# Optimization experiments

Measured on AMD Instinct MI355X. Metric: run time of the kernel, lower is better.

## Reference

```python
import jax, jax.numpy as jnp
import numpy as np

SIGMA = 5.67e-8  # Stefan-Boltzmann constant
NX = 13
N = NX * NX  # 169 nodes
B = 131072


def _build_matrices(L=0.1, thickness=0.001, board_k=15.0, emis=0.8):
    dx = L / (NX - 1)
    dy = L / (NX - 1)
    GLx = thickness * board_k * dy / dx
    GLy = thickness * board_k * dx / dy
    GR = 2.0 * dx * dy * emis
    iface = {0, NX - 1, NX * NX - 1, NX * NX - NX}
    K = np.zeros((N, N), dtype=np.float32)
    for j in range(NX):
        for i in range(NX):
            idn = i + NX * j
            if idn in iface:
                K[idn, idn] = 1.0
            else:
                gii = 0.0
                if i + 1 < NX:
                    K[idn, idn + 1] = -GLx  # east
                    gii += GLx
                if i - 1 >= 0:
                    K[idn, idn - 1] = -GLx  # west
                    gii += GLx
                if j + 1 < NX:
                    K[idn, idn + NX] = -GLx  # north (original code uses -GLx here too)
                    gii += GLy
                if j - 1 >= 0:
                    K[idn, idn - NX] = -GLx  # south (original code uses -GLx here too)
                    gii += GLy
                K[idn, idn] = gii
    e = np.full(N, GR, dtype=np.float32)
    for t in iface:
        e[t] = 0.0
    return jnp.asarray(K), jnp.asarray(e)


def setup_inputs() -> dict:
    key = jax.random.key(0)
    k1, k2, k3, k4 = jax.random.split(key, 4)
    # realistic temperatures (K) and heat loads (W)
    outputs = 270.0 + 60.0 * jax.random.uniform(k1, (B, NX, NX), dtype=jnp.float32)
    heaters = 0.5 * jax.random.uniform(k2, (B, NX, NX), dtype=jnp.float32)
    interfaces = 0.5 * jax.random.uniform(k3, (B, NX, NX), dtype=jnp.float32)
    Tenv = 270.0 + 30.0 * jax.random.uniform(k4, (B, 1), dtype=jnp.float32)
    K, e_diag = _build_matrices()
    return {"outputs": outputs, "heaters": heaters, "interfaces": interfaces,
            "Tenv": Tenv, "K": K, "e_diag": e_diag}


def reference(outputs, heaters, interfaces, Tenv, K, e_diag):
    b = outputs.shape[0]
    T = outputs.reshape(b, -1)                    # [B, 169]
    Q = heaters.reshape(b, -1) + interfaces.reshape(b, -1)  # [B, 169]
    # original computes K @ T_nodes_x_batch; batch-major equivalent is T @ K^T
    conduction = jnp.einsum('bn,mn->bm', T, K)    # [B, 169]
    radiation = SIGMA * e_diag[None, :] * (T ** 4 - Tenv ** 4)  # Tenv [B,1] broadcasts
    excess = conduction + radiation - Q
    return jnp.mean(jnp.abs(excess))
```

## Files before the change

kernel.cpp:

```cpp
#include <hip/hip_runtime.h>
#include <math.h>
#include <stdint.h>


#define SIGMA_F 5.67e-8f

constexpr int BLOCK = 256;
constexpr int TILE  = 2048;
constexpr int THALO = 16;
constexpr int TWIN  = TILE + 2 * THALO;

typedef float f4b __attribute__((ext_vector_type(4), aligned(16)));

static __device__ __forceinline__ void gl_lds16(const float* g, float* l) {
    __builtin_amdgcn_global_load_lds(
        (const __attribute__((address_space(1))) void*)g,
        (__attribute__((address_space(3))) void*)l, 16, 0, 0);
}

__global__ __launch_bounds__(256) void fused_residual_v9(
    const float* __restrict__ T,
    const float* __restrict__ H,
    const float* __restrict__ F,
    const float* __restrict__ Tenv,
    const float* __restrict__ K,
    const float* __restrict__ Ediag,
    float* __restrict__ partials,
    int total,
    int ntiles)
{
    __shared__ float sT[2][TWIN];
    __shared__ float sH[2][TILE];
    __shared__ float sF[2][TILE];
    __shared__ unsigned sTab[184];
    __shared__ float sred[BLOCK / 64];

    const float GLx = -K[1 * 169 + 2];
    const float GRs = SIGMA_F * Ediag[1];
    const int tid = (int)threadIdx.x;

    if (tid < 184) {
        int m = (tid < 169) ? tid : tid - 169;
        int ii = m % 13;
        unsigned cW = (ii > 0)  ? 1u : 0u;
        unsigned cE = (ii < 12) ? 1u : 0u;
        unsigned cN = (m < 156) ? 1u : 0u;
        unsigned cS = (m >= 13) ? 1u : 0u;
        sTab[tid] = cW | (cE << 8) | (cN << 16) | (cS << 24);
    }

    const int nb  = (int)gridDim.x;
    const int bid = (int)blockIdx.x;
    const int qd  = ntiles / nb, rem = ntiles % nb;
    const int t0  = bid * qd + (bid < rem ? bid : rem);
    const int nt  = qd + (bid < rem ? 1 : 0);

    float acc = 0.0f;

    auto STAGE = [&](int buf, int tile) {
        const int gb = tile * TILE;
        #pragma unroll
        for (int k = 0; k < 3; ++k) {
            const int c = tid + k * BLOCK;
            if (c < TWIN / 4) {
                int src = gb - THALO + c * 4;
                src = src < 0 ? 0 : src;
                src = src > total - 4 ? total - 4 : src;
                gl_lds16(T + src, &sT[buf][c * 4]);
            }
        }
        #pragma unroll
        for (int k = 0; k < 2; ++k) {
            const int c = tid + k * BLOCK;
            gl_lds16(H + gb + c * 4, &sH[buf][c * 4]);
            gl_lds16(F + gb + c * 4, &sF[buf][c * 4]);
        }
    };

    if (nt > 0) {
        STAGE(0, t0);
        __syncthreads();
        int cur = 0;
        for (int k = 0; k < nt; ++k) {
            if (k + 1 < nt) STAGE(cur ^ 1, t0 + k + 1);

            const int tb = (t0 + k) * TILE;
            const int e0 = tb + tid * 8;
            const int lb = THALO + tid * 8;
            const float* __restrict__ Tb = &sT[cur][0];

            f4b a0 = *(const f4b*)&Tb[lb];
            f4b a1 = *(const f4b*)&Tb[lb + 4];
            float s0 = Tb[lb - 13];
            f4b sA = *(const f4b*)&Tb[lb - 12];
            f4b sB = *(const f4b*)&Tb[lb - 8];
            float n0 = Tb[lb + 13], n1 = Tb[lb + 14], n2 = Tb[lb + 15];
            f4b nA = *(const f4b*)&Tb[lb + 16];
            float n7 = Tb[lb + 20];
            float tw = Tb[lb - 1], te = Tb[lb + 8];
            f4b h0v = *(const f4b*)&sH[cur][tid * 8];
            f4b h1v = *(const f4b*)&sH[cur][tid * 8 + 4];
            f4b f0v = *(const f4b*)&sF[cur][tid * 8];
            f4b f1v = *(const f4b*)&sF[cur][tid * 8 + 4];

            const float tC[8] = {a0.x, a0.y, a0.z, a0.w, a1.x, a1.y, a1.z, a1.w};
            const float sv[8] = {s0, sA.x, sA.y, sA.z, sA.w, sB.x, sB.y, sB.z};
            const float nv[8] = {n0, n1, n2, nA.x, nA.y, nA.z, nA.w, n7};
            const float qv[8] = {h0v.x + f0v.x, h0v.y + f0v.y,
                                 h0v.z + f0v.z, h0v.w + f0v.w,
                                 h1v.x + f1v.x, h1v.y + f1v.y,
                                 h1v.z + f1v.z, h1v.w + f1v.w};

            const unsigned ue = (unsigned)e0;
            const unsigned b0 = ue / 169u;
            const int m0 = (int)(ue - b0 * 169u);

            float tvA = Tenv[b0];
            float tvB = tvA;
            if (m0 >= 162) tvB = Tenv[b0 + 1];
            const float tv4A = (tvA * tvA) * (tvA * tvA);
            const float tv4B = (tvB * tvB) * (tvB * tvB);

            #pragma unroll
            for (int j = 0; j < 8; ++j) {
                const unsigned w = sTab[m0 + j];
                const float mW = (float)(w & 0xffu);
                const float mE = (float)((w >> 8) & 0xffu);
                const float mN = (float)((w >> 16) & 0xffu);
                const float mS = (float)(w >> 24);

                const float t  = tC[j];
                const float twv = (j == 0) ? tw : tC[j - 1];
                const float tev = (j == 7) ? te : tC[j + 1];
                float s = mW * twv;
                s = fmaf(mE, tev, s);
                s = fmaf(mN, nv[j], s);
                s = fmaf(mS, sv[j], s);
                const float nn = (mW + mE) + (mN + mS);
                const float q  = qv[j];
                const float tv4 = (m0 + j >= 169) ? tv4B : tv4A;
                const float t2 = t * t;
                const float d  = fmaf(t2, t2, -tv4);
                const float core = fmaf(GLx, fmaf(nn, t, -s), fmaf(GRs, d, -q));
                const float ex = (nn == 2.0f) ? (t - q) : core;
                acc += fabsf(ex);
            }

            __syncthreads();
            cur ^= 1;
        }
    }

    for (int e = ntiles * TILE + bid * BLOCK + tid; e < total;
         e += nb * BLOCK) {
        unsigned b = (unsigned)e / 169u;
        int m = e - (int)b * 169;
        int ii = m % 13;
        bool cE = (ii < 12), cW = (ii > 0), cN = (m < 156), cS = (m >= 13);
        bool ifc = (m == 0) | (m == 12) | (m == 156) | (m == 168);
        float t  = T[e];
        float s  = (cE ? T[e + 1] : 0.0f) + (cW ? T[e - 1] : 0.0f)
                 + (cN ? T[e + 13] : 0.0f) + (cS ? T[e - 13] : 0.0f);
        float nn = (float)((int)cE + (int)cW + (int)cN + (int)cS);
        float tv = Tenv[b];
        float tv4 = (tv * tv) * (tv * tv);
        float t2 = t * t, t4 = t2 * t2;
        float qq = H[e] + F[e];
        float ex = ifc ? (t - qq) : (GLx * (nn * t - s) + GRs * (t4 - tv4) - qq);
        acc += fabsf(ex);
    }

    #pragma unroll
    for (int off = 32; off > 0; off >>= 1)
        acc += __shfl_down(acc, off, 64);
    const int lane = tid & 63;
    const int wid  = tid >> 6;
    if (lane == 0) sred[wid] = acc;
    __syncthreads();
    if (tid == 0) {
        float s = 0.0f;
        #pragma unroll
        for (int w = 0; w < BLOCK / 64; ++w) s += sred[w];
        partials[bid] = s;
    }
}

__global__ __launch_bounds__(256) void finalize_kernel(
    const float* __restrict__ partials, int n,
    float* __restrict__ out, float inv_total)
{
    __shared__ float sred[BLOCK / 64];
    float acc = 0.0f;
    for (int i = (int)threadIdx.x; i < n; i += BLOCK) acc += partials[i];
    #pragma unroll
    for (int off = 32; off > 0; off >>= 1)
        acc += __shfl_down(acc, off, 64);
    int lane = threadIdx.x & 63;
    int wid  = threadIdx.x >> 6;
    if (lane == 0) sred[wid] = acc;
    __syncthreads();
    if (threadIdx.x == 0) {
        float s = 0.0f;
        #pragma unroll
        for (int w = 0; w < BLOCK / 64; ++w) s += sred[w];
        out[0] = s * inv_total;
    }
}

extern "C" void kernel_launch(void* const* d_in, const int* in_sizes, int n_in,
                              void* d_out, int out_size, void* d_ws, size_t ws_size,
                              hipStream_t stream) {
    const float* T    = (const float*)d_in[0];
    const float* H    = (const float*)d_in[1];
    const float* F    = (const float*)d_in[2];
    const float* Tenv = (const float*)d_in[3];
    const float* K    = (const float*)d_in[4];
    const float* E    = (const float*)d_in[5];
    float* out      = (float*)d_out;
    float* partials = (float*)d_ws;

    const int total  = in_sizes[0];
    const int ntiles = total / TILE;

    int grid = 768;
    if (grid > ntiles) grid = ntiles > 0 ? ntiles : 1;
    if ((size_t)grid * sizeof(float) > ws_size) grid = (int)(ws_size / sizeof(float));
    if (grid < 1) grid = 1;

    fused_residual_v9<<<grid, BLOCK, 0, stream>>>(T, H, F, Tenv, K, E, partials,
                                                  total, ntiles);

    const float inv_total = 1.0f / (float)total;
    finalize_kernel<<<1, BLOCK, 0, stream>>>(partials, grid, out, inv_total);
}
```

Baseline: 268.3 us.

## Give each wavefront its own double-buffered tile with vmcnt waits instead of block barriers

Each of the four wavefronts in a block now owns a private 512-element double-buffered LDS slice. It stages T (with halo), H, F and the needed Tenv values by async global-to-LDS loads, and waits on vmcnt counters instead of block-wide __syncthreads. Tenv is also prefetched into LDS rather than read with scattered global loads, and tiles are strided across all wavefronts in the grid. The aim is to remove block-level barrier stalls and let each wave overlap its own loads with compute. The cost is more halo overhead per element and reliance on hand-written waitcnt ordering.

```diff
diff --git a/kernel.cpp b/kernel.cpp
--- a/kernel.cpp
+++ b/kernel.cpp
@@ -1,24 +1,31 @@
 #include <hip/hip_runtime.h>
 #include <math.h>
-#include <stdint.h>
 
 
 #define SIGMA_F 5.67e-8f
 
 constexpr int BLOCK = 256;
-constexpr int TILE  = 2048;
-constexpr int THALO = 16;
-constexpr int TWIN  = TILE + 2 * THALO;
+constexpr int TILE  = 512;
+constexpr int HOFF  = 544;
+constexpr int FOFF  = 1056;
+constexpr int EOFF  = 1568;
+constexpr int SLICE = 1632;
+constexpr int WSTR  = 2 * SLICE;
 
 typedef float f4b __attribute__((ext_vector_type(4), aligned(16)));
 
-static __device__ __forceinline__ void gl_lds16(const float* g, float* l) {
+static __device__ __forceinline__ void gl16(const float* g, float* l) {
     __builtin_amdgcn_global_load_lds(
         (const __attribute__((address_space(1))) void*)g,
         (__attribute__((address_space(3))) void*)l, 16, 0, 0);
 }
-
-__global__ __launch_bounds__(256) void fused_residual_v9(
+static __device__ __forceinline__ void gl4(const float* g, float* l) {
+    __builtin_amdgcn_global_load_lds(
+        (const __attribute__((address_space(1))) void*)g,
+        (__attribute__((address_space(3))) void*)l, 4, 0, 0);
+}
+
+__global__ __launch_bounds__(256) void fused_residual_v12(
     const float* __restrict__ T,
     const float* __restrict__ H,
     const float* __restrict__ F,
@@ -26,18 +33,18 @@
     const float* __restrict__ K,
     const float* __restrict__ Ediag,
     float* __restrict__ partials,
-    int total,
-    int ntiles)
+    int total)
 {
-    __shared__ float sT[2][TWIN];
-    __shared__ float sH[2][TILE];
-    __shared__ float sF[2][TILE];
+    __shared__ float    S[4 * WSTR];
     __shared__ unsigned sTab[184];
-    __shared__ float sred[BLOCK / 64];
+    __shared__ float    sred[4];
+
+    const int tid  = (int)threadIdx.x;
+    const int lane = tid & 63;
+    const int wid  = tid >> 6;
 
     const float GLx = -K[1 * 169 + 2];
     const float GRs = SIGMA_F * Ediag[1];
-    const int tid = (int)threadIdx.x;
 
     if (tid < 184) {
         int m = (tid < 169) ? tid : tid - 169;
@@ -49,139 +56,137 @@
         sTab[tid] = cW | (cE << 8) | (cN << 16) | (cS << 24);
     }
 
-    const int nb  = (int)gridDim.x;
-    const int bid = (int)blockIdx.x;
-    const int qd  = ntiles / nb, rem = ntiles % nb;
-    const int t0  = bid * qd + (bid < rem ? bid : rem);
-    const int nt  = qd + (bid < rem ? 1 : 0);
-
     float acc = 0.0f;
-
-    auto STAGE = [&](int buf, int tile) {
-        const int gb = tile * TILE;
-        #pragma unroll
-        for (int k = 0; k < 3; ++k) {
-            const int c = tid + k * BLOCK;
-            if (c < TWIN / 4) {
-                int src = gb - THALO + c * 4;
-                src = src < 0 ? 0 : src;
-                src = src > total - 4 ? total - 4 : src;
-                gl_lds16(T + src, &sT[buf][c * 4]);
-            }
+    const int ntiles = total / TILE;
+
+    if (blockIdx.x == 0) {
+        for (int e = ntiles * TILE + tid; e < total; e += BLOCK) {
+            unsigned bb = (unsigned)e / 169u;
+            int m = e - (int)bb * 169;
+            int ii = m % 13;
+            bool cE = (ii < 12), cW = (ii > 0), cN = (m < 156), cS = (m >= 13);
+            bool ifc = (m == 0) | (m == 12) | (m == 156) | (m == 168);
+            float t  = T[e];
+            float s  = (cE ? T[e + 1] : 0.0f) + (cW ? T[e - 1] : 0.0f)
+                     + (cN ? T[e + 13] : 0.0f) + (cS ? T[e - 13] : 0.0f);
+            float nn = (float)((int)cE + (int)cW + (int)cN + (int)cS);
+            float tv = Tenv[bb];
+            float tv4 = (tv * tv) * (tv * tv);
+            float t2 = t * t, t4 = t2 * t2;
+            float qq = H[e] + F[e];
+            acc += fabsf(ifc ? (t - qq)
+                             : (GLx * (nn * t - s) + GRs * (t4 - tv4) - qq));
         }
-        #pragma unroll
-        for (int k = 0; k < 2; ++k) {
-            const int c = tid + k * BLOCK;
-            gl_lds16(H + gb + c * 4, &sH[buf][c * 4]);
-            gl_lds16(F + gb + c * 4, &sF[buf][c * 4]);
+    }
+    __syncthreads();
+
+    const int nw    = (int)gridDim.x * 4;
+    const int tile0 = (int)blockIdx.x * 4 + wid;
+    const int wbase = wid * WSTR;
+    const int Bm1   = total / 169 - 1;
+    const int smax  = total - 4;
+
+    auto STAGE = [&](int buf, int t) {
+        const int tb = t * TILE;
+        float* sl = &S[wbase + buf * SLICE];
+        const int l4 = 4 * lane;
+        int s0 = tb - 16 + l4;  s0 = s0 < 0 ? 0 : s0;
+        int s2 = tb + 272 + l4; s2 = s2 > smax ? smax : s2;
+        gl16(T + s0,            sl + l4);
+        gl16(T + tb + 240 + l4, sl + 256 + l4);
+        gl16(T + s2,            sl + 288 + l4);
+        gl16(H + tb + l4,       sl + HOFF + l4);
+        gl16(H + tb + 256 + l4, sl + HOFF + 256 + l4);
+        gl16(F + tb + l4,       sl + FOFF + l4);
+        gl16(F + tb + 256 + l4, sl + FOFF + 256 + l4);
+        int bw = (int)((unsigned)tb / 169u) + lane;
+        bw = bw > Bm1 ? Bm1 : bw;
+        gl4(Tenv + bw, sl + EOFF + lane);
+    };
+
+    int buf = 0;
+    if (tile0 < ntiles) STAGE(0, tile0);
+
+    for (int t = tile0; t < ntiles; t += nw) {
+        const int tn = t + nw;
+        if (tn < ntiles) {
+            STAGE(buf ^ 1, tn);
+            asm volatile("s_waitcnt vmcnt(8)" ::: "memory");
+        } else {
+            asm volatile("s_waitcnt vmcnt(0)" ::: "memory");
         }
-    };
-
-    if (nt > 0) {
-        STAGE(0, t0);
-        __syncthreads();
-        int cur = 0;
-        for (int k = 0; k < nt; ++k) {
-            if (k + 1 < nt) STAGE(cur ^ 1, t0 + k + 1);
-
-            const int tb = (t0 + k) * TILE;
-            const int e0 = tb + tid * 8;
-            const int lb = THALO + tid * 8;
-            const float* __restrict__ Tb = &sT[cur][0];
-
-            f4b a0 = *(const f4b*)&Tb[lb];
-            f4b a1 = *(const f4b*)&Tb[lb + 4];
-            float s0 = Tb[lb - 13];
-            f4b sA = *(const f4b*)&Tb[lb - 12];
-            f4b sB = *(const f4b*)&Tb[lb - 8];
-            float n0 = Tb[lb + 13], n1 = Tb[lb + 14], n2 = Tb[lb + 15];
-            f4b nA = *(const f4b*)&Tb[lb + 16];
-            float n7 = Tb[lb + 20];
-            float tw = Tb[lb - 1], te = Tb[lb + 8];
-            f4b h0v = *(const f4b*)&sH[cur][tid * 8];
-            f4b h1v = *(const f4b*)&sH[cur][tid * 8 + 4];
-            f4b f0v = *(const f4b*)&sF[cur][tid * 8];
-            f4b f1v = *(const f4b*)&sF[cur][tid * 8 + 4];
-
-            const float tC[8] = {a0.x, a0.y, a0.z, a0.w, a1.x, a1.y, a1.z, a1.w};
-            const float sv[8] = {s0, sA.x, sA.y, sA.z, sA.w, sB.x, sB.y, sB.z};
-            const float nv[8] = {n0, n1, n2, nA.x, nA.y, nA.z, nA.w, n7};
-            const float qv[8] = {h0v.x + f0v.x, h0v.y + f0v.y,
-                                 h0v.z + f0v.z, h0v.w + f0v.w,
-                                 h1v.x + f1v.x, h1v.y + f1v.y,
-                                 h1v.z + f1v.z, h1v.w + f1v.w};
-
-            const unsigned ue = (unsigned)e0;
-            const unsigned b0 = ue / 169u;
-            const int m0 = (int)(ue - b0 * 169u);
-
-            float tvA = Tenv[b0];
-            float tvB = tvA;
-            if (m0 >= 162) tvB = Tenv[b0 + 1];
-            const float tv4A = (tvA * tvA) * (tvA * tvA);
-            const float tv4B = (tvB * tvB) * (tvB * tvB);
-
-            #pragma unroll
-            for (int j = 0; j < 8; ++j) {
-                const unsigned w = sTab[m0 + j];
-                const float mW = (float)(w & 0xffu);
-                const float mE = (float)((w >> 8) & 0xffu);
-                const float mN = (float)((w >> 16) & 0xffu);
-                const float mS = (float)(w >> 24);
-
-                const float t  = tC[j];
-                const float twv = (j == 0) ? tw : tC[j - 1];
-                const float tev = (j == 7) ? te : tC[j + 1];
-                float s = mW * twv;
-                s = fmaf(mE, tev, s);
-                s = fmaf(mN, nv[j], s);
-                s = fmaf(mS, sv[j], s);
-                const float nn = (mW + mE) + (mN + mS);
-                const float q  = qv[j];
-                const float tv4 = (m0 + j >= 169) ? tv4B : tv4A;
-                const float t2 = t * t;
-                const float d  = fmaf(t2, t2, -tv4);
-                const float core = fmaf(GLx, fmaf(nn, t, -s), fmaf(GRs, d, -q));
-                const float ex = (nn == 2.0f) ? (t - q) : core;
-                acc += fabsf(ex);
-            }
-
-            __syncthreads();
-            cur ^= 1;
+        __builtin_amdgcn_sched_barrier(0);
+
+        const int tb = t * TILE;
+        const float* sl = &S[wbase + buf * SLICE];
+        const int lb = 16 + lane * 8;
+
+        f4b a0 = *(const f4b*)&sl[lb];
+        f4b a1 = *(const f4b*)&sl[lb + 4];
+        float sv[8], nv[8];
+        #pragma unroll
+        for (int j = 0; j < 8; ++j) sv[j] = sl[lb - 13 + j];
+        #pragma unroll
+        for (int j = 0; j < 8; ++j) nv[j] = sl[lb + 13 + j];
+        const float tw0 = sl[lb - 1];
+        const float te7 = sl[lb + 8];
+        f4b h0 = *(const f4b*)&sl[HOFF + lane * 8];
+        f4b h1 = *(const f4b*)&sl[HOFF + lane * 8 + 4];
+        f4b f0 = *(const f4b*)&sl[FOFF + lane * 8];
+        f4b f1 = *(const f4b*)&sl[FOFF + lane * 8 + 4];
+
+        const int e0 = tb + lane * 8;
+        const unsigned b0 = (unsigned)e0 / 169u;
+        const int m0 = e0 - (int)(b0 * 169u);
+        const int b0w = (int)((unsigned)tb / 169u);
+        const int relb = (int)b0 - b0w;
+        const float tvA = sl[EOFF + relb];
+        const float tvB = sl[EOFF + relb + 1];
+        const float tv4A = (tvA * tvA) * (tvA * tvA);
+        const float tv4B = (tvB * tvB) * (tvB * tvB);
+
+        const float tCv[8] = {a0.x, a0.y, a0.z, a0.w, a1.x, a1.y, a1.z, a1.w};
+        const float tWv[8] = {tw0, a0.x, a0.y, a0.z, a0.w, a1.x, a1.y, a1.z};
+        const float tEv[8] = {a0.y, a0.z, a0.w, a1.x, a1.y, a1.z, a1.w, te7};
+        const float qv[8]  = {h0.x + f0.x, h0.y + f0.y, h0.z + f0.z, h0.w + f0.w,
+                              h1.x + f1.x, h1.y + f1.y, h1.z + f1.z, h1.w + f1.w};
+
+        #pragma unroll
+        for (int j = 0; j < 8; ++j) {
+            const unsigned w = sTab[m0 + j];
+            const float mW = (float)(w & 0xffu);
+            const float mE = (float)((w >> 8) & 0xffu);
+            const float mN = (float)((w >> 16) & 0xffu);
+            const float mS = (float)(w >> 24);
+
+            const float t1 = tCv[j];
+            float s = mW * tWv[j];
+            s = fmaf(mE, tEv[j], s);
+            s = fmaf(mN, nv[j], s);
+            s = fmaf(mS, sv[j], s);
+            const float nn = (mW + mE) + (mN + mS);
+            const float q  = qv[j];
+            const float tv4 = (m0 + j >= 169) ? tv4B : tv4A;
+            const float t2 = t1 * t1;
+            const float d  = fmaf(t2, t2, -tv4);
+            const float core = fmaf(GLx, fmaf(nn, t1, -s), fmaf(GRs, d, -q));
+            const float ex = (nn == 2.0f) ? (t1 - q) : core;
+            acc += fabsf(ex);
         }
-    }
-
-    for (int e = ntiles * TILE + bid * BLOCK + tid; e < total;
-         e += nb * BLOCK) {
-        unsigned b = (unsigned)e / 169u;
-        int m = e - (int)b * 169;
-        int ii = m % 13;
-        bool cE = (ii < 12), cW = (ii > 0), cN = (m < 156), cS = (m >= 13);
-        bool ifc = (m == 0) | (m == 12) | (m == 156) | (m == 168);
-        float t  = T[e];
-        float s  = (cE ? T[e + 1] : 0.0f) + (cW ? T[e - 1] : 0.0f)
-                 + (cN ? T[e + 13] : 0.0f) + (cS ? T[e - 13] : 0.0f);
-        float nn = (float)((int)cE + (int)cW + (int)cN + (int)cS);
-        float tv = Tenv[b];
-        float tv4 = (tv * tv) * (tv * tv);
-        float t2 = t * t, t4 = t2 * t2;
-        float qq = H[e] + F[e];
-        float ex = ifc ? (t - qq) : (GLx * (nn * t - s) + GRs * (t4 - tv4) - qq);
-        acc += fabsf(ex);
+
+        buf ^= 1;
     }
 
     #pragma unroll
     for (int off = 32; off > 0; off >>= 1)
         acc += __shfl_down(acc, off, 64);
-    const int lane = tid & 63;
-    const int wid  = tid >> 6;
     if (lane == 0) sred[wid] = acc;
     __syncthreads();
     if (tid == 0) {
         float s = 0.0f;
         #pragma unroll
-        for (int w = 0; w < BLOCK / 64; ++w) s += sred[w];
-        partials[bid] = s;
+        for (int w = 0; w < 4; ++w) s += sred[w];
+        partials[blockIdx.x] = s;
     }
 }
 
@@ -219,16 +224,16 @@
     float* out      = (float*)d_out;
     float* partials = (float*)d_ws;
 
-    const int total  = in_sizes[0];
+    const int total = in_sizes[0];
+
+    int grid = 768;
     const int ntiles = total / TILE;
-
-    int grid = 768;
-    if (grid > ntiles) grid = ntiles > 0 ? ntiles : 1;
+    if (grid > ntiles && ntiles > 0) grid = (ntiles + 3) / 4;
     if ((size_t)grid * sizeof(float) > ws_size) grid = (int)(ws_size / sizeof(float));
     if (grid < 1) grid = 1;
 
-    fused_residual_v9<<<grid, BLOCK, 0, stream>>>(T, H, F, Tenv, K, E, partials,
-                                                  total, ntiles);
+    fused_residual_v12<<<grid, BLOCK, 0, stream>>>(T, H, F, Tenv, K, E, partials,
+                                                   total);
 
     const float inv_total = 1.0f / (float)total;
     finalize_kernel<<<1, BLOCK, 0, stream>>>(partials, grid, out, inv_total);
```

Result: faster. 262.6 us (-2.1%).
